# Optimization experiments

Hardware: AMD Instinct MI355X
Metric: run time of the kernel (lower is better)

## Reference

```python
import jax, jax.numpy as jnp
import numpy as np

N = 400000      # active voxels
C_IN = 64
C_OUT = 64
GRID = 128      # voxel grid extent per axis
K = 3           # kernel size -> 27 offsets
EPS = 1e-5      # BatchNorm eps


def _build_neighbor_map():
    """Kernel map for stride-1 sparse conv: nmap[k, i] = input voxel index at
    coords[i] + offset[k], or -1 if that voxel is inactive / out of bounds."""
    rng = np.random.default_rng(0)
    raw = rng.integers(0, GRID, size=(3 * N // 2, 3))
    keys = (raw[:, 0] * GRID + raw[:, 1]) * GRID + raw[:, 2]
    ukeys = np.unique(keys)
    assert len(ukeys) >= N
    ukeys = ukeys[:N]  # sorted voxel keys of the N active sites
    x = ukeys // (GRID * GRID)
    y = (ukeys // GRID) % GRID
    z = ukeys % GRID
    r = np.arange(-(K // 2), K // 2 + 1)
    offs = np.stack(np.meshgrid(r, r, r, indexing="ij"), -1).reshape(-1, 3)
    nmap = np.full((offs.shape[0], N), -1, dtype=np.int32)
    for k, (dx, dy, dz) in enumerate(offs):
        nx, ny, nz = x + dx, y + dy, z + dz
        inb = (nx >= 0) & (nx < GRID) & (ny >= 0) & (ny < GRID) & (nz >= 0) & (nz < GRID)
        qk = (nx * GRID + ny) * GRID + nz
        pos = np.clip(np.searchsorted(ukeys, qk), 0, N - 1)
        hit = inb & (ukeys[pos] == qk)
        nmap[k] = np.where(hit, pos, -1).astype(np.int32)
    return jnp.asarray(nmap)


def setup_inputs() -> dict:
    key = jax.random.key(0)
    k1, k2 = jax.random.split(key)
    features = jax.random.normal(k1, (N, C_IN), jnp.float32)
    neighbor_map = _build_neighbor_map()  # [27, N] int32
    fan_in = C_IN * K ** 3
    weight = jax.random.normal(k2, (K ** 3, C_IN, C_OUT), jnp.float32) * (1.0 / np.sqrt(fan_in))
    gamma = jnp.ones((C_OUT,), jnp.float32)
    beta = jnp.zeros((C_OUT,), jnp.float32)
    return {"features": features, "neighbor_map": neighbor_map,
            "weight": weight, "gamma": gamma, "beta": beta}


def _sparse_conv(features, neighbor_map, weight):
    # gather-GEMM-scatter, accumulated over the 27 kernel offsets via scan
    n = features.shape[0]
    def step(acc, inp):
        idx, w_k = inp                                    # [N], [C_in, C_out]
        safe = jnp.maximum(idx, 0)
        g = jnp.where((idx >= 0)[:, None], features[safe], 0.0)  # gather [N, C_in]
        return acc + g @ w_k, None
    init = jnp.zeros((n, weight.shape[-1]), features.dtype)
    out, _ = jax.lax.scan(step, init, (neighbor_map, weight))
    return out


def reference(features, neighbor_map, weight, gamma, beta):
    out = _sparse_conv(features, neighbor_map, weight)   # [N, C_out]
    mean = out.mean(axis=0)                              # BatchNorm (training stats)
    var = out.var(axis=0)
    y = (out - mean) * jax.lax.rsqrt(var + EPS) * gamma + beta
    return jnp.maximum(y, 0.0)                           # ReLU
```

## Files before the change

kernel.cpp:

```cpp
#include <hip/hip_runtime.h>

#define NVOX 400000
#define K27 27
#define EPS_ 1e-5f

typedef short short8 __attribute__((ext_vector_type(8)));
typedef float floatx4 __attribute__((ext_vector_type(4)));
typedef unsigned int uintx4 __attribute__((ext_vector_type(4)));

__device__ __forceinline__ unsigned int pack2bf(float a, float b) {
    unsigned int ua = __builtin_bit_cast(unsigned int, a);
    unsigned int ub = __builtin_bit_cast(unsigned int, b);
    ua += 0x7fffu + ((ua >> 16) & 1u);
    ub += 0x7fffu + ((ub >> 16) & 1u);
    return (ua >> 16) | (ub & 0xffff0000u);
}

__global__ void prep_kernel(const float* __restrict__ w,
                            const float* __restrict__ feat,
                            unsigned short* __restrict__ feat_bf,
                            unsigned short* __restrict__ wt,
                            float* __restrict__ sums,
                            int fb) {
    const int b = blockIdx.x;
    const int t = threadIdx.x;
    if (b < fb) {
#pragma unroll
        for (int r = 0; r < 4; ++r) {
            const int i0 = b * 8192 + r * 2048 + t * 8;
            const floatx4* s = (const floatx4*)(feat + i0);
            const floatx4 f0 = s[0], f1 = s[1];
            uintx4 v;
            v[0] = pack2bf(f0[0], f0[1]); v[1] = pack2bf(f0[2], f0[3]);
            v[2] = pack2bf(f1[0], f1[1]); v[3] = pack2bf(f1[2], f1[3]);
            *(uintx4*)(feat_bf + i0) = v;
        }
    } else if (b < fb + 32) {
        for (int g = (b - fb) * 256 + t; g < K27 * 64 * 64; g += 32 * 256) {
            const int k = g >> 12, r = g & 4095, co = r >> 6, ci = r & 63;
            unsigned int u =
                __builtin_bit_cast(unsigned int, w[(k << 12) + (ci << 6) + co]);
            u += 0x7fffu + ((u >> 16) & 1u);
            wt[g] = (unsigned short)(u >> 16);
        }
    } else {
        if (t < 128) sums[t] = 0.0f;
    }
}

template <bool BF16FEAT>
__launch_bounds__(256)
__global__ void conv_mfma(const float* __restrict__ feat,
                          const unsigned short* __restrict__ feat_bf,
                          const int* __restrict__ nmap,
                          const unsigned short* __restrict__ wt,
                          float* __restrict__ out,
                          float* __restrict__ sums) {
    __shared__ __align__(16) unsigned short a_tile[128 * 64];
    __shared__ __align__(16) unsigned short b_tile[64 * 64];
    __shared__ int idx_lds[K27 * 128];
    __shared__ float cstat[128];

    const int tid  = threadIdx.x;
    const int wv   = tid >> 6;
    const int lane = tid & 63;
    const int m    = lane & 15;
    const int q    = lane >> 4;
    const int base = blockIdx.x * 128;

    for (int j = tid; j < K27 * 128; j += 256)
        idx_lds[j] = nmap[(j >> 7) * NVOX + base + (j & 127)];
    if (tid < 128) cstat[tid] = 0.0f;
    __syncthreads();

    const int gc = tid & 7;
    int arow[4], apos[4];
#pragma unroll
    for (int j = 0; j < 4; ++j) {
        const int c = tid + 256 * j;
        arow[j] = c >> 3;
        apos[j] = (arow[j] * 8 + (gc ^ (arow[j] & 7))) * 8;
    }
    int bsrc[2], bpos[2];
#pragma unroll
    for (int j = 0; j < 2; ++j) {
        const int c = tid + 256 * j;
        bsrc[j] = c * 8;
        bpos[j] = ((c >> 3) * 8 + ((c & 7) ^ ((c >> 3) & 7))) * 8;
    }
    int row_a[2];
#pragma unroll
    for (int mt = 0; mt < 2; ++mt) row_a[mt] = wv * 32 + mt * 16 + m;

    floatx4 acc[2][4];
#pragma unroll
    for (int mt = 0; mt < 2; ++mt)
#pragma unroll
        for (int nt = 0; nt < 4; ++nt)
            acc[mt][nt] = (floatx4){0.f, 0.f, 0.f, 0.f};

    short8 aregA[4], bregA[2];
    short8 aregB[4], bregB[2];
    int idxA[4], idxB[4];

#define FETCH_SET(areg, breg, idxc, kk)                                       \
    do {                                                                      \
        _Pragma("unroll") for (int j = 0; j < 4; ++j)                         \
            idxc[j] = idx_lds[(kk) * 128 + arow[j]];                          \
        _Pragma("unroll") for (int j = 0; j < 4; ++j) {                       \
            if (idxc[j] >= 0) {                                               \
                if (BF16FEAT) {                                               \
                    areg[j] = *(const short8*)(                               \
                        feat_bf + (size_t)idxc[j] * 64 + gc * 8);             \
                } else {                                                      \
                    const floatx4* sp = (const floatx4*)(                     \
                        feat + (size_t)idxc[j] * 64 + gc * 8);                \
                    const floatx4 f0 = sp[0], f1 = sp[1];                     \
                    uintx4 v;                                                 \
                    v[0] = pack2bf(f0[0], f0[1]);                             \
                    v[1] = pack2bf(f0[2], f0[3]);                             \
                    v[2] = pack2bf(f1[0], f1[1]);                             \
                    v[3] = pack2bf(f1[2], f1[3]);                             \
                    areg[j] = __builtin_bit_cast(short8, v);                  \
                }                                                             \
            }                                                                 \
        }                                                                     \
        _Pragma("unroll") for (int j = 0; j < 2; ++j)                         \
            breg[j] = *(const short8*)(wt + (kk) * 4096 + bsrc[j]);           \
    } while (0)

#define STAGE_SET(areg, breg, idxc)                                           \
    do {                                                                      \
        _Pragma("unroll") for (int j = 0; j < 4; ++j)                         \
            if (idxc[j] >= 0) *(short8*)(a_tile + apos[j]) = areg[j];         \
        _Pragma("unroll") for (int j = 0; j < 2; ++j)                         \
            *(short8*)(b_tile + bpos[j]) = breg[j];                           \
    } while (0)

#define COMPUTE(kk)                                                           \
    do {                                                                      \
        bool am[2];                                                           \
        _Pragma("unroll") for (int mt = 0; mt < 2; ++mt)                      \
            am[mt] = idx_lds[(kk) * 128 + row_a[mt]] >= 0;                    \
        _Pragma("unroll") for (int kb = 0; kb < 2; ++kb) {                    \
            short8 af[2], bf[4];                                              \
            _Pragma("unroll") for (int mt = 0; mt < 2; ++mt) {                \
                af[mt] = *(const short8*)(                                    \
                    a_tile + (row_a[mt] * 8 +                                 \
                              ((kb * 4 + q) ^ (row_a[mt] & 7))) * 8);         \
                if (!am[mt]) af[mt] = (short8){0, 0, 0, 0, 0, 0, 0, 0};       \
            }                                                                 \
            _Pragma("unroll") for (int nt = 0; nt < 4; ++nt) {                \
                const int row = nt * 16 + m;                                  \
                bf[nt] = *(const short8*)(                                    \
                    b_tile + (row * 8 + ((kb * 4 + q) ^ (row & 7))) * 8);     \
            }                                                                 \
            _Pragma("unroll") for (int mt = 0; mt < 2; ++mt)                  \
                _Pragma("unroll") for (int nt = 0; nt < 4; ++nt)              \
                    acc[mt][nt] = __builtin_amdgcn_mfma_f32_16x16x32_bf16(    \
                        af[mt], bf[nt], acc[mt][nt], 0, 0, 0);                \
        }                                                                     \
    } while (0)

    FETCH_SET(aregA, bregA, idxA, 0);

    for (int kk = 0; kk < K27; kk += 2) {
        if (kk + 1 < K27) FETCH_SET(aregB, bregB, idxB, kk + 1);
        __syncthreads();
        STAGE_SET(aregA, bregA, idxA);
        __syncthreads();
        COMPUTE(kk);
        if (kk + 1 >= K27) break;
        if (kk + 2 < K27) FETCH_SET(aregA, bregA, idxA, kk + 2);
        __syncthreads();
        STAGE_SET(aregB, bregB, idxB);
        __syncthreads();
        COMPUTE(kk + 1);
    }
#undef FETCH_SET
#undef STAGE_SET
#undef COMPUTE

#pragma unroll
    for (int nt = 0; nt < 4; ++nt) {
        const int col = nt * 16 + m;
        float s = 0.f, s2 = 0.f;
#pragma unroll
        for (int mt = 0; mt < 2; ++mt) {
            const int row0 = base + wv * 32 + mt * 16 + q * 4;
#pragma unroll
            for (int i = 0; i < 4; ++i) {
                const float v = acc[mt][nt][i];
                s += v;
                s2 += v * v;
                out[(size_t)(row0 + i) * 64 + col] = v;
            }
        }
        atomicAdd(&cstat[col], s);
        atomicAdd(&cstat[64 + col], s2);
    }
    __syncthreads();
    if (tid < 128) atomicAdd(&sums[tid], cstat[tid]);
}

__global__ void bn_apply(float* __restrict__ out, const float* __restrict__ sums,
                         const float* __restrict__ gamma,
                         const float* __restrict__ beta) {
    __shared__ float sc[64];
    __shared__ float sh[64];
    const int tid = threadIdx.x;
    if (tid < 64) {
        const float inv_n = 1.0f / (float)NVOX;
        const float mean = sums[tid] * inv_n;
        const float var  = sums[64 + tid] * inv_n - mean * mean;
        const float g    = gamma[tid] * rsqrtf(var + EPS_);
        sc[tid] = g;
        sh[tid] = beta[tid] - mean * g;
    }
    __syncthreads();
    const int cg = (tid & 15) * 4;
    floatx4 scale, shift;
#pragma unroll
    for (int j = 0; j < 4; ++j) {
        scale[j] = sc[cg + j];
        shift[j] = sh[cg + j];
    }
    floatx4* p = (floatx4*)out;
    const int total4 = NVOX * 16;
    for (int i = blockIdx.x * 256 + tid; i < total4; i += gridDim.x * 256) {
        floatx4 v = p[i] * scale + shift;
#pragma unroll
        for (int j = 0; j < 4; ++j) v[j] = v[j] > 0.f ? v[j] : 0.f;
        p[i] = v;
    }
}

extern "C" void kernel_launch(void* const* d_in, const int* in_sizes, int n_in,
                              void* d_out, int out_size, void* d_ws, size_t ws_size,
                              hipStream_t stream) {
    const float* feat  = (const float*)d_in[0];
    const int*   nmap  = (const int*)d_in[1];
    const float* w     = (const float*)d_in[2];
    const float* gamma = (const float*)d_in[3];
    const float* beta  = (const float*)d_in[4];
    float* out = (float*)d_out;

    const size_t FEATB = (size_t)NVOX * 64 * 2;
    const size_t WTB   = (size_t)K27 * 64 * 64 * 2;
    const int conv_blocks = NVOX / 128;

    if (ws_size >= FEATB + WTB + 512) {
        unsigned short* feat_bf = (unsigned short*)d_ws;
        unsigned short* wt      = (unsigned short*)((char*)d_ws + FEATB);
        float* sums             = (float*)((char*)d_ws + FEATB + WTB);
        prep_kernel<<<dim3(3158), dim3(256), 0, stream>>>(
            w, feat, feat_bf, wt, sums, 3125);
        conv_mfma<true><<<dim3(conv_blocks), dim3(256), 0, stream>>>(
            feat, feat_bf, nmap, wt, out, sums);
        bn_apply<<<dim3(1024), dim3(256), 0, stream>>>(out, sums, gamma, beta);
    } else {
        unsigned short* wt = (unsigned short*)d_ws;
        float* sums        = (float*)((char*)d_ws + WTB);
        prep_kernel<<<dim3(33), dim3(256), 0, stream>>>(
            w, feat, nullptr, wt, sums, 0);
        conv_mfma<false><<<dim3(conv_blocks), dim3(256), 0, stream>>>(
            feat, nullptr, nmap, wt, out, sums);
        bn_apply<<<dim3(1024), dim3(256), 0, stream>>>(out, sums, gamma, beta);
    }
}
```

Baseline: 471.5 us.

## Load MFMA operands directly from global memory, dropping LDS staging and barriers

The gather-GEMM loop no longer stages A and B tiles through shared memory. Each lane now loads its MFMA fragments straight from global memory into registers, double-buffered across kernel offsets, which removes the LDS writes, the swizzled LDS reads and four block barriers per pair of offsets. In exchange, weights are loaded redundantly by every wave rather than once per block, more fragment registers are live at once, and the per-lane loads are 16-byte chunks at strided offsets instead of cooperative row loads.

```diff
diff --git a/kernel.cpp b/kernel.cpp
--- a/kernel.cpp
+++ b/kernel.cpp
@@ -56,8 +56,6 @@
                           const unsigned short* __restrict__ wt,
                           float* __restrict__ out,
                           float* __restrict__ sums) {
-    __shared__ __align__(16) unsigned short a_tile[128 * 64];
-    __shared__ __align__(16) unsigned short b_tile[64 * 64];
     __shared__ int idx_lds[K27 * 128];
     __shared__ float cstat[128];
 
@@ -73,21 +71,6 @@
     if (tid < 128) cstat[tid] = 0.0f;
     __syncthreads();
 
-    const int gc = tid & 7;
-    int arow[4], apos[4];
-#pragma unroll
-    for (int j = 0; j < 4; ++j) {
-        const int c = tid + 256 * j;
-        arow[j] = c >> 3;
-        apos[j] = (arow[j] * 8 + (gc ^ (arow[j] & 7))) * 8;
-    }
-    int bsrc[2], bpos[2];
-#pragma unroll
-    for (int j = 0; j < 2; ++j) {
-        const int c = tid + 256 * j;
-        bsrc[j] = c * 8;
-        bpos[j] = ((c >> 3) * 8 + ((c & 7) ^ ((c >> 3) & 7))) * 8;
-    }
     int row_a[2];
 #pragma unroll
     for (int mt = 0; mt < 2; ++mt) row_a[mt] = wv * 32 + mt * 16 + m;
@@ -99,86 +82,61 @@
         for (int nt = 0; nt < 4; ++nt)
             acc[mt][nt] = (floatx4){0.f, 0.f, 0.f, 0.f};
 
-    short8 aregA[4], bregA[2];
-    short8 aregB[4], bregB[2];
-    int idxA[4], idxB[4];
-
-#define FETCH_SET(areg, breg, idxc, kk)                                       \
+    short8 aA[2][2], bA[4][2];
+    short8 aB[2][2], bB[4][2];
+
+#define FETCH(aset, bset, kk)                                                 \
     do {                                                                      \
-        _Pragma("unroll") for (int j = 0; j < 4; ++j)                         \
-            idxc[j] = idx_lds[(kk) * 128 + arow[j]];                          \
-        _Pragma("unroll") for (int j = 0; j < 4; ++j) {                       \
-            if (idxc[j] >= 0) {                                               \
+        _Pragma("unroll") for (int mt = 0; mt < 2; ++mt) {                    \
+            const int ix = idx_lds[(kk) * 128 + row_a[mt]];                   \
+            _Pragma("unroll") for (int kb = 0; kb < 2; ++kb)                  \
+                aset[mt][kb] = (short8){0, 0, 0, 0, 0, 0, 0, 0};              \
+            if (ix >= 0) {                                                    \
                 if (BF16FEAT) {                                               \
-                    areg[j] = *(const short8*)(                               \
-                        feat_bf + (size_t)idxc[j] * 64 + gc * 8);             \
+                    const unsigned short* ap =                                \
+                        feat_bf + (size_t)ix * 64 + q * 8;                    \
+                    _Pragma("unroll") for (int kb = 0; kb < 2; ++kb)          \
+                        aset[mt][kb] = *(const short8*)(ap + kb * 32);        \
                 } else {                                                      \
-                    const floatx4* sp = (const floatx4*)(                     \
-                        feat + (size_t)idxc[j] * 64 + gc * 8);                \
-                    const floatx4 f0 = sp[0], f1 = sp[1];                     \
-                    uintx4 v;                                                 \
-                    v[0] = pack2bf(f0[0], f0[1]);                             \
-                    v[1] = pack2bf(f0[2], f0[3]);                             \
-                    v[2] = pack2bf(f1[0], f1[1]);                             \
-                    v[3] = pack2bf(f1[2], f1[3]);                             \
-                    areg[j] = __builtin_bit_cast(short8, v);                  \
+                    const float* fp = feat + (size_t)ix * 64 + q * 8;         \
+                    _Pragma("unroll") for (int kb = 0; kb < 2; ++kb) {        \
+                        const floatx4 f0 = *(const floatx4*)(fp + kb * 32);   \
+                        const floatx4 f1 =                                    \
+                            *(const floatx4*)(fp + kb * 32 + 4);              \
+                        uintx4 v;                                             \
+                        v[0] = pack2bf(f0[0], f0[1]);                         \
+                        v[1] = pack2bf(f0[2], f0[3]);                         \
+                        v[2] = pack2bf(f1[0], f1[1]);                         \
+                        v[3] = pack2bf(f1[2], f1[3]);                         \
+                        aset[mt][kb] = __builtin_bit_cast(short8, v);         \
+                    }                                                         \
                 }                                                             \
             }                                                                 \
         }                                                                     \
-        _Pragma("unroll") for (int j = 0; j < 2; ++j)                         \
-            breg[j] = *(const short8*)(wt + (kk) * 4096 + bsrc[j]);           \
+        const unsigned short* bp = wt + (kk) * 4096 + m * 64 + q * 8;         \
+        _Pragma("unroll") for (int nt = 0; nt < 4; ++nt)                      \
+            _Pragma("unroll") for (int kb = 0; kb < 2; ++kb)                  \
+                bset[nt][kb] = *(const short8*)(bp + nt * 1024 + kb * 32);    \
     } while (0)
 
-#define STAGE_SET(areg, breg, idxc)                                           \
+#define COMPUTE(aset, bset)                                                   \
     do {                                                                      \
-        _Pragma("unroll") for (int j = 0; j < 4; ++j)                         \
-            if (idxc[j] >= 0) *(short8*)(a_tile + apos[j]) = areg[j];         \
-        _Pragma("unroll") for (int j = 0; j < 2; ++j)                         \
-            *(short8*)(b_tile + bpos[j]) = breg[j];                           \
-    } while (0)
-
-#define COMPUTE(kk)                                                           \
-    do {                                                                      \
-        bool am[2];                                                           \
-        _Pragma("unroll") for (int mt = 0; mt < 2; ++mt)                      \
-            am[mt] = idx_lds[(kk) * 128 + row_a[mt]] >= 0;                    \
-        _Pragma("unroll") for (int kb = 0; kb < 2; ++kb) {                    \
-            short8 af[2], bf[4];                                              \
-            _Pragma("unroll") for (int mt = 0; mt < 2; ++mt) {                \
-                af[mt] = *(const short8*)(                                    \
-                    a_tile + (row_a[mt] * 8 +                                 \
-                              ((kb * 4 + q) ^ (row_a[mt] & 7))) * 8);         \
-                if (!am[mt]) af[mt] = (short8){0, 0, 0, 0, 0, 0, 0, 0};       \
-            }                                                                 \
-            _Pragma("unroll") for (int nt = 0; nt < 4; ++nt) {                \
-                const int row = nt * 16 + m;                                  \
-                bf[nt] = *(const short8*)(                                    \
-                    b_tile + (row * 8 + ((kb * 4 + q) ^ (row & 7))) * 8);     \
-            }                                                                 \
+        _Pragma("unroll") for (int kb = 0; kb < 2; ++kb)                      \
             _Pragma("unroll") for (int mt = 0; mt < 2; ++mt)                  \
                 _Pragma("unroll") for (int nt = 0; nt < 4; ++nt)              \
                     acc[mt][nt] = __builtin_amdgcn_mfma_f32_16x16x32_bf16(    \
-                        af[mt], bf[nt], acc[mt][nt], 0, 0, 0);                \
-        }                                                                     \
+                        aset[mt][kb], bset[nt][kb], acc[mt][nt], 0, 0, 0);    \
     } while (0)
 
-    FETCH_SET(aregA, bregA, idxA, 0);
-
+    FETCH(aA, bA, 0);
     for (int kk = 0; kk < K27; kk += 2) {
-        if (kk + 1 < K27) FETCH_SET(aregB, bregB, idxB, kk + 1);
-        __syncthreads();
-        STAGE_SET(aregA, bregA, idxA);
-        __syncthreads();
-        COMPUTE(kk);
+        if (kk + 1 < K27) FETCH(aB, bB, kk + 1);
+        COMPUTE(aA, bA);
         if (kk + 1 >= K27) break;
-        if (kk + 2 < K27) FETCH_SET(aregA, bregA, idxA, kk + 2);
-        __syncthreads();
-        STAGE_SET(aregB, bregB, idxB);
-        __syncthreads();
-        COMPUTE(kk + 1);
-    }
-#undef FETCH_SET
-#undef STAGE_SET
+        if (kk + 2 < K27) FETCH(aA, bA, kk + 2);
+        COMPUTE(aB, bB);
+    }
+#undef FETCH
 #undef COMPUTE
 
 #pragma unroll
```

After: 597.1 us. 1.27x slower.

## Stage gathered features directly to LDS with double-buffered async loads

Applied to the files above, without the earlier changes.

Replaces the register-staged gather and LDS store with global_load_lds direct-to-LDS transfers into double-buffered A/B tiles. Inactive neighbours now point at a zeroed row in workspace, so the per-row masking and the idx_lds preload are no longer needed. Blocks are also remapped so that consecutive voxel tiles land on the same XCD. The goal is to drop VGPR staging, cut barriers, and overlap the next offset's gather with the current MFMA work, at the cost of doubling LDS tile usage and reading nmap from global memory inside the loop.

```diff
diff --git a/kernel.cpp b/kernel.cpp
--- a/kernel.cpp
+++ b/kernel.cpp
@@ -16,11 +16,18 @@
     return (ua >> 16) | (ub & 0xffff0000u);
 }
 
+__device__ __forceinline__ void gload_lds16(const void* g, void* l) {
+    __builtin_amdgcn_global_load_lds(
+        (const __attribute__((address_space(1))) void*)g,
+        (__attribute__((address_space(3))) void*)l, 16, 0, 0);
+}
+
 __global__ void prep_kernel(const float* __restrict__ w,
                             const float* __restrict__ feat,
                             unsigned short* __restrict__ feat_bf,
                             unsigned short* __restrict__ wt,
                             float* __restrict__ sums,
+                            float* __restrict__ zrow,
                             int fb) {
     const int b = blockIdx.x;
     const int t = threadIdx.x;
@@ -45,6 +52,7 @@
         }
     } else {
         if (t < 128) sums[t] = 0.0f;
+        else if (zrow && t < 136) zrow[t - 128] = 0.0f;
     }
 }
 
@@ -54,11 +62,11 @@
                           const unsigned short* __restrict__ feat_bf,
                           const int* __restrict__ nmap,
                           const unsigned short* __restrict__ wt,
+                          const unsigned short* __restrict__ zrow,
                           float* __restrict__ out,
                           float* __restrict__ sums) {
-    __shared__ __align__(16) unsigned short a_tile[128 * 64];
-    __shared__ __align__(16) unsigned short b_tile[64 * 64];
-    __shared__ int idx_lds[K27 * 128];
+    __shared__ __align__(16) unsigned short a_tile[2][128 * 64];
+    __shared__ __align__(16) unsigned short b_tile[2][64 * 64];
     __shared__ float cstat[128];
 
     const int tid  = threadIdx.x;
@@ -66,28 +74,16 @@
     const int lane = tid & 63;
     const int m    = lane & 15;
     const int q    = lane >> 4;
-    const int base = blockIdx.x * 128;
-
-    for (int j = tid; j < K27 * 128; j += 256)
-        idx_lds[j] = nmap[(j >> 7) * NVOX + base + (j & 127)];
+
+    const int nwg = gridDim.x;
+    const int q8 = nwg >> 3, r8 = nwg & 7;
+    const int xcd = blockIdx.x & 7, lin = blockIdx.x >> 3;
+    const int wg =
+        (xcd < r8 ? xcd * (q8 + 1) : r8 * (q8 + 1) + (xcd - r8) * q8) + lin;
+    const int base = wg * 128;
+
     if (tid < 128) cstat[tid] = 0.0f;
-    __syncthreads();
-
-    const int gc = tid & 7;
-    int arow[4], apos[4];
-#pragma unroll
-    for (int j = 0; j < 4; ++j) {
-        const int c = tid + 256 * j;
-        arow[j] = c >> 3;
-        apos[j] = (arow[j] * 8 + (gc ^ (arow[j] & 7))) * 8;
-    }
-    int bsrc[2], bpos[2];
-#pragma unroll
-    for (int j = 0; j < 2; ++j) {
-        const int c = tid + 256 * j;
-        bsrc[j] = c * 8;
-        bpos[j] = ((c >> 3) * 8 + ((c & 7) ^ ((c >> 3) & 7))) * 8;
-    }
+
     int row_a[2];
 #pragma unroll
     for (int mt = 0; mt < 2; ++mt) row_a[mt] = wv * 32 + mt * 16 + m;
@@ -99,61 +95,39 @@
         for (int nt = 0; nt < 4; ++nt)
             acc[mt][nt] = (floatx4){0.f, 0.f, 0.f, 0.f};
 
-    short8 aregA[4], bregA[2];
-    short8 aregB[4], bregB[2];
-    int idxA[4], idxB[4];
-
-#define FETCH_SET(areg, breg, idxc, kk)                                       \
+#define STAGE_G(bufidx, kk)                                                   \
     do {                                                                      \
-        _Pragma("unroll") for (int j = 0; j < 4; ++j)                         \
-            idxc[j] = idx_lds[(kk) * 128 + arow[j]];                          \
         _Pragma("unroll") for (int j = 0; j < 4; ++j) {                       \
-            if (idxc[j] >= 0) {                                               \
-                if (BF16FEAT) {                                               \
-                    areg[j] = *(const short8*)(                               \
-                        feat_bf + (size_t)idxc[j] * 64 + gc * 8);             \
-                } else {                                                      \
-                    const floatx4* sp = (const floatx4*)(                     \
-                        feat + (size_t)idxc[j] * 64 + gc * 8);                \
-                    const floatx4 f0 = sp[0], f1 = sp[1];                     \
-                    uintx4 v;                                                 \
-                    v[0] = pack2bf(f0[0], f0[1]);                             \
-                    v[1] = pack2bf(f0[2], f0[3]);                             \
-                    v[2] = pack2bf(f1[0], f1[1]);                             \
-                    v[3] = pack2bf(f1[2], f1[3]);                             \
-                    areg[j] = __builtin_bit_cast(short8, v);                  \
-                }                                                             \
-            }                                                                 \
+            const int blk = j * 4 + wv;                                       \
+            const int row = blk * 8 + (lane >> 3);                            \
+            const int gc  = (lane & 7) ^ (row & 7);                           \
+            const int ix  = nmap[(size_t)(kk) * NVOX + base + row];           \
+            const unsigned short* src =                                       \
+                (ix >= 0) ? feat_bf + (size_t)ix * 64 + gc * 8 : zrow;        \
+            gload_lds16(src, a_tile[bufidx] + blk * 512);                     \
         }                                                                     \
-        _Pragma("unroll") for (int j = 0; j < 2; ++j)                         \
-            breg[j] = *(const short8*)(wt + (kk) * 4096 + bsrc[j]);           \
+        _Pragma("unroll") for (int j = 0; j < 2; ++j) {                       \
+            const int blk = j * 4 + wv;                                       \
+            const int row = blk * 8 + (lane >> 3);                            \
+            const int gc  = (lane & 7) ^ (row & 7);                           \
+            gload_lds16(wt + (kk)*4096 + row * 64 + gc * 8,                   \
+                        b_tile[bufidx] + blk * 512);                          \
+        }                                                                     \
     } while (0)
 
-#define STAGE_SET(areg, breg, idxc)                                           \
+#define COMPUTE(bufidx)                                                       \
     do {                                                                      \
-        _Pragma("unroll") for (int j = 0; j < 4; ++j)                         \
-            if (idxc[j] >= 0) *(short8*)(a_tile + apos[j]) = areg[j];         \
-        _Pragma("unroll") for (int j = 0; j < 2; ++j)                         \
-            *(short8*)(b_tile + bpos[j]) = breg[j];                           \
-    } while (0)
-
-#define COMPUTE(kk)                                                           \
-    do {                                                                      \
-        bool am[2];                                                           \
-        _Pragma("unroll") for (int mt = 0; mt < 2; ++mt)                      \
-            am[mt] = idx_lds[(kk) * 128 + row_a[mt]] >= 0;                    \
         _Pragma("unroll") for (int kb = 0; kb < 2; ++kb) {                    \
             short8 af[2], bf[4];                                              \
-            _Pragma("unroll") for (int mt = 0; mt < 2; ++mt) {                \
+            _Pragma("unroll") for (int mt = 0; mt < 2; ++mt)                  \
                 af[mt] = *(const short8*)(                                    \
-                    a_tile + (row_a[mt] * 8 +                                 \
-                              ((kb * 4 + q) ^ (row_a[mt] & 7))) * 8);         \
-                if (!am[mt]) af[mt] = (short8){0, 0, 0, 0, 0, 0, 0, 0};       \
-            }                                                                 \
+                    a_tile[bufidx] +                                          \
+                    (row_a[mt] * 8 + ((kb * 4 + q) ^ (row_a[mt] & 7))) * 8);  \
             _Pragma("unroll") for (int nt = 0; nt < 4; ++nt) {                \
                 const int row = nt * 16 + m;                                  \
                 bf[nt] = *(const short8*)(                                    \
-                    b_tile + (row * 8 + ((kb * 4 + q) ^ (row & 7))) * 8);     \
+                    b_tile[bufidx] +                                          \
+                    (row * 8 + ((kb * 4 + q) ^ (row & 7))) * 8);              \
             }                                                                 \
             _Pragma("unroll") for (int mt = 0; mt < 2; ++mt)                  \
                 _Pragma("unroll") for (int nt = 0; nt < 4; ++nt)              \
@@ -162,23 +136,65 @@
         }                                                                     \
     } while (0)
 
-    FETCH_SET(aregA, bregA, idxA, 0);
-
-    for (int kk = 0; kk < K27; kk += 2) {
-        if (kk + 1 < K27) FETCH_SET(aregB, bregB, idxB, kk + 1);
+    if constexpr (BF16FEAT) {
         __syncthreads();
-        STAGE_SET(aregA, bregA, idxA);
+        STAGE_G(0, 0);
         __syncthreads();
-        COMPUTE(kk);
-        if (kk + 1 >= K27) break;
-        if (kk + 2 < K27) FETCH_SET(aregA, bregA, idxA, kk + 2);
-        __syncthreads();
-        STAGE_SET(aregB, bregB, idxB);
-        __syncthreads();
-        COMPUTE(kk + 1);
-    }
-#undef FETCH_SET
-#undef STAGE_SET
+        for (int kk = 0; kk < K27; kk += 2) {
+            if (kk + 1 < K27) STAGE_G(1, kk + 1);
+            COMPUTE(0);
+            __syncthreads();
+            if (kk + 1 >= K27) break;
+            if (kk + 2 < K27) STAGE_G(0, kk + 2);
+            COMPUTE(1);
+            __syncthreads();
+        }
+    } else {
+        for (int kk = 0; kk < K27; ++kk) {
+            short8 areg[4], breg[2];
+            int arow[4];
+#pragma unroll
+            for (int j = 0; j < 4; ++j) {
+                const int c = tid + 256 * j;
+                arow[j] = c >> 3;
+                const int gcs = c & 7;
+                const int ix = nmap[(size_t)kk * NVOX + base + arow[j]];
+                areg[j] = (short8){0, 0, 0, 0, 0, 0, 0, 0};
+                if (ix >= 0) {
+                    const float* fp = feat + (size_t)ix * 64 + gcs * 8;
+                    const floatx4 f0 = *(const floatx4*)fp;
+                    const floatx4 f1 = *(const floatx4*)(fp + 4);
+                    uintx4 v;
+                    v[0] = pack2bf(f0[0], f0[1]); v[1] = pack2bf(f0[2], f0[3]);
+                    v[2] = pack2bf(f1[0], f1[1]); v[3] = pack2bf(f1[2], f1[3]);
+                    areg[j] = __builtin_bit_cast(short8, v);
+                }
+            }
+#pragma unroll
+            for (int j = 0; j < 2; ++j) {
+                const int c = tid + 256 * j;
+                breg[j] = *(const short8*)(wt + kk * 4096 + c * 8);
+            }
+            __syncthreads();
+#pragma unroll
+            for (int j = 0; j < 4; ++j) {
+                const int c = tid + 256 * j;
+                *(short8*)(a_tile[0] +
+                           (arow[j] * 8 + ((c & 7) ^ (arow[j] & 7))) * 8) =
+                    areg[j];
+            }
+#pragma unroll
+            for (int j = 0; j < 2; ++j) {
+                const int c = tid + 256 * j;
+                const int br = c >> 3;
+                *(short8*)(b_tile[0] + (br * 8 + ((c & 7) ^ (br & 7))) * 8) =
+                    breg[j];
+            }
+            __syncthreads();
+            COMPUTE(0);
+        }
+    }
+#undef STAGE_G
 #undef COMPUTE
 
 #pragma unroll
@@ -249,22 +265,23 @@
     const size_t WTB   = (size_t)K27 * 64 * 64 * 2;
     const int conv_blocks = NVOX / 128;
 
-    if (ws_size >= FEATB + WTB + 512) {
+    if (ws_size >= FEATB + WTB + 512 + 128) {
         unsigned short* feat_bf = (unsigned short*)d_ws;
         unsigned short* wt      = (unsigned short*)((char*)d_ws + FEATB);
         float* sums             = (float*)((char*)d_ws + FEATB + WTB);
+        float* zrow             = (float*)((char*)d_ws + FEATB + WTB + 512);
         prep_kernel<<<dim3(3158), dim3(256), 0, stream>>>(
-            w, feat, feat_bf, wt, sums, 3125);
+            w, feat, feat_bf, wt, sums, zrow, 3125);
         conv_mfma<true><<<dim3(conv_blocks), dim3(256), 0, stream>>>(
-            feat, feat_bf, nmap, wt, out, sums);
+            feat, feat_bf, nmap, wt, (const unsigned short*)zrow, out, sums);
         bn_apply<<<dim3(1024), dim3(256), 0, stream>>>(out, sums, gamma, beta);
     } else {
         unsigned short* wt = (unsigned short*)d_ws;
         float* sums        = (float*)((char*)d_ws + WTB);
         prep_kernel<<<dim3(33), dim3(256), 0, stream>>>(
-            w, feat, nullptr, wt, sums, 0);
+            w, feat, nullptr, wt, sums, nullptr, 0);
         conv_mfma<false><<<dim3(conv_blocks), dim3(256), 0, stream>>>(
-            feat, nullptr, nmap, wt, out, sums);
+            feat, nullptr, nmap, wt, nullptr, out, sums);
         bn_apply<<<dim3(1024), dim3(256), 0, stream>>>(out, sums, gamma, beta);
     }
 }
```

After: 444.0 us. -5.8%, faster.
